# Kernel tuning notes

Measured on AMD Instinct MI355X. Metric: run time of the kernel, lower is better.

## Reference

```python
import jax, jax.numpy as jnp
import numpy as np

B, S, C, HD = 2, 4096, 2048, 128
H = C // HD  # 16 heads
EPS = 1.1920929e-07  # torch RMSNorm default eps for float32 (finfo.eps)


def _make_rope(seq_len, head_dim):
    # Standard RoPE 2x2 rotation matrices: [1, S, 1, head_dim//2, 2, 2]
    half = head_dim // 2
    freqs = 1.0 / (10000.0 ** (np.arange(0, half, dtype=np.float32) / half))
    ang = np.arange(seq_len, dtype=np.float32)[:, None] * freqs[None, :]  # [S, half]
    cos, sin = np.cos(ang), np.sin(ang)
    rot = np.stack([np.stack([cos, -sin], axis=-1),
                    np.stack([sin, cos], axis=-1)], axis=-2)  # [S, half, 2, 2]
    return jnp.asarray(rot[None, :, None])  # [1, S, 1, half, 2, 2]


def setup_inputs() -> dict:
    key = jax.random.key(0)
    ks = jax.random.split(key, 9)
    sc = 1.0 / np.sqrt(C)
    return {
        "x": jax.random.normal(ks[0], (B, S, C), jnp.float32),
        "rope": _make_rope(S, HD),
        "wq": jax.random.normal(ks[1], (C, C), jnp.float32) * sc,
        "bq": jax.random.normal(ks[2], (C,), jnp.float32) * 0.01,
        "wk": jax.random.normal(ks[3], (C, C), jnp.float32) * sc,
        "bk": jax.random.normal(ks[4], (C,), jnp.float32) * 0.01,
        "wv": jax.random.normal(ks[5], (C, C), jnp.float32) * sc,
        "bv": jax.random.normal(ks[6], (C,), jnp.float32) * 0.01,
        "q_norm_w": jnp.ones((HD,), jnp.float32),
        "k_norm_w": jnp.ones((HD,), jnp.float32),
    }


def _rmsnorm(t, w):
    t32 = t.astype(jnp.float32)
    inv = jax.lax.rsqrt(jnp.mean(t32 * t32, axis=-1, keepdims=True) + EPS)
    return (t32 * inv * w).astype(t.dtype)


def _apply_rotary(t, rope):
    # t: [B, S, H, HD] -> pairs [B, S, H, HD//2, 1, 2]; rope: [1, S, 1, HD//2, 2, 2]
    t32 = t.reshape(*t.shape[:-1], HD // 2, 1, 2).astype(jnp.float32)
    out = (rope * t32).sum(axis=-1)  # [B, S, H, HD//2, 2]
    return out.reshape(t.shape).astype(t.dtype)


def reference(x, rope, wq, bq, wk, bk, wv, bv, q_norm_w, k_norm_w):
    # QKV projections (torch Linear: x @ W^T + b)
    q = (jnp.einsum('bsc,oc->bso', x, wq) + bq).reshape(B, S, H, HD)
    k = (jnp.einsum('bsc,oc->bso', x, wk) + bk).reshape(B, S, H, HD)
    v = (jnp.einsum('bsc,oc->bso', x, wv) + bv).reshape(B, S, H, HD)
    # Per-head RMSNorm on q, k (in float32, cast back), then rotary
    q = _apply_rotary(_rmsnorm(q, q_norm_w), rope)
    k = _apply_rotary(_rmsnorm(k, k_norm_w), rope)
    return (q, k, v)
```

## Files before the change

### kernel.cpp

```cpp
#include <hip/hip_runtime.h>


#define M_DIM 8192
#define N_DIM 6144
#define K_DIM 2048
#define NKT 32
#define EPS_RMS 1.1920929e-07f

typedef __bf16 bf16x8 __attribute__((ext_vector_type(8)));
typedef float f32x4 __attribute__((ext_vector_type(4)));

__device__ __forceinline__ void gload16(const void* g, void* l) {
  __builtin_amdgcn_global_load_lds(
      (const __attribute__((address_space(1))) unsigned int*)g,
      (__attribute__((address_space(3))) unsigned int*)l, 16, 0, 0);
}

__device__ __forceinline__ unsigned short f2bf(float f) {
  union { float f; unsigned u; } x; x.f = f;
  unsigned r = x.u + 0x7FFFu + ((x.u >> 16) & 1u);
  return (unsigned short)(r >> 16);
}

__global__ void __launch_bounds__(256) cvt_kernel(const float* __restrict__ s,
                                                  unsigned short* __restrict__ d, int n4) {
  int i = blockIdx.x * blockDim.x + threadIdx.x;
  const int stride = gridDim.x * blockDim.x;
  for (; i < n4; i += stride) {
    const float4 v = reinterpret_cast<const float4*>(s)[i];
    ushort4 o;
    o.x = f2bf(v.x); o.y = f2bf(v.y); o.z = f2bf(v.z); o.w = f2bf(v.w);
    reinterpret_cast<ushort4*>(d)[i] = o;
  }
}

#define LDS4(ARR, BASE, OFF) (*(const f32x4*)((const char*)(ARR) + (BASE) + (OFF)))

#define SGB_DS(N)   __builtin_amdgcn_sched_group_barrier(0x100, (N), 0)
#define SGB_MFMA(N) __builtin_amdgcn_sched_group_barrier(0x8, (N), 0)

#define MFMA_PH(MH, NH)                                                              \
  {                                                                                  \
    _Pragma("unroll")                                                                \
    for (int mf4 = 0; mf4 < 4; ++mf4) {                                              \
      _Pragma("unroll")                                                              \
      for (int nf2 = 0; nf2 < 2; ++nf2) {                                            \
        f32x4& c = acc[(MH) * 4 + mf4][(NH) * 2 + nf2];                              \
        c = __builtin_amdgcn_mfma_f32_16x16x32_bf16(                                 \
            __builtin_bit_cast(bf16x8, Af[mf4][0]),                                  \
            __builtin_bit_cast(bf16x8, Bf[NH][nf2][0]), c, 0, 0, 0);                 \
        c = __builtin_amdgcn_mfma_f32_16x16x32_bf16(                                 \
            __builtin_bit_cast(bf16x8, Af[mf4][1]),                                  \
            __builtin_bit_cast(bf16x8, Bf[NH][nf2][1]), c, 0, 0, 0);                 \
      }                                                                              \
    }                                                                                \
  }

__global__ void __launch_bounds__(512, 2) gemm_fused(
    const unsigned short* __restrict__ xbf, const unsigned short* __restrict__ wbf,
    const float* __restrict__ rope,
    const float* __restrict__ bq, const float* __restrict__ bk, const float* __restrict__ bv,
    const float* __restrict__ qnw, const float* __restrict__ knw,
    float* __restrict__ dout) {
  const int id = blockIdx.x;
  const int xcd = id & 7;
  const int j = id >> 3;
  const int bm = (xcd << 2) | (j & 3);
  const int bn = j >> 2;
  const int m0 = bm << 8, n0 = bn << 8;
  const int tid = threadIdx.x;
  const int w = tid >> 6, l = tid & 63;
  const int l15 = l & 15, lhi = l >> 4;
  const int wr = w >> 2, wc = w & 3;

  __shared__ __align__(16) unsigned short As[32768];
  __shared__ __align__(16) unsigned short Bs[32768];

  const int srow = tid >> 3;
  const int schunk = (tid & 7) ^ (srow & 7);
  const unsigned short* aSrc = xbf + ((size_t)(m0 + srow) << 11) + (schunk << 3);
  const unsigned short* bSrc = wbf + ((size_t)(n0 + srow) << 11) + (schunk << 3);
  char* aDst = (char*)As + (w << 10);
  char* bDst = (char*)Bs + (w << 10);

#define STA(KT, Q) gload16(aSrc + ((size_t)(Q) << 17) + ((KT) << 6), aDst + ((((KT) & 1) << 15) + ((Q) << 13)))
#define STB(KT, Q) gload16(bSrc + ((size_t)(Q) << 17) + ((KT) << 6), bDst + ((((KT) & 1) << 15) + ((Q) << 13)))

  const int sl0 = ((lhi ^ (l15 & 7)) << 4);
  const int sl1 = (((lhi + 4) ^ (l15 & 7)) << 4);
  unsigned a0 = (wr << 14) + (l15 << 7) + sl0;
  unsigned a1 = (wr << 14) + (l15 << 7) + sl1;
  unsigned b0 = (wc << 13) + (l15 << 7) + sl0;
  unsigned b1 = (wc << 13) + (l15 << 7) + sl1;

  f32x4 acc[8][4];
#pragma unroll
  for (int i = 0; i < 8; ++i)
#pragma unroll
    for (int jj = 0; jj < 4; ++jj) acc[i][jj] = (f32x4){0.f, 0.f, 0.f, 0.f};

  f32x4 Af[4][2];
  f32x4 Bf[2][2][2];

  STA(0, 0); STA(0, 2);
  STB(0, 0); STB(0, 1); STB(0, 2); STB(0, 3);
  STA(0, 1); STA(0, 3);
  asm volatile("s_waitcnt vmcnt(2)" ::: "memory");
  __builtin_amdgcn_s_barrier();
  asm volatile("" ::: "memory");

  for (int kt = 0; kt < NKT; ++kt) {
    const bool notLast = (kt < NKT - 1);
    Af[0][0] = LDS4(As, a0, 0);        Af[0][1] = LDS4(As, a1, 0);
    Bf[0][0][0] = LDS4(Bs, b0, 0);     Bf[0][0][1] = LDS4(Bs, b1, 0);
    Bf[0][1][0] = LDS4(Bs, b0, 2048);  Bf[0][1][1] = LDS4(Bs, b1, 2048);
    Af[1][0] = LDS4(As, a0, 2048);     Af[1][1] = LDS4(As, a1, 2048);
    Af[2][0] = LDS4(As, a0, 4096);     Af[2][1] = LDS4(As, a1, 4096);
    Af[3][0] = LDS4(As, a0, 6144);     Af[3][1] = LDS4(As, a1, 6144);
    Bf[1][0][0] = LDS4(Bs, b0, 4096);  Bf[1][0][1] = LDS4(Bs, b1, 4096);
    Bf[1][1][0] = LDS4(Bs, b0, 6144);  Bf[1][1][1] = LDS4(Bs, b1, 6144);
    if (notLast) {
      STA(kt + 1, 0); STA(kt + 1, 2);
      STB(kt + 1, 0); STB(kt + 1, 1); STB(kt + 1, 2); STB(kt + 1, 3);
    }
    __builtin_amdgcn_s_setprio(1);
    MFMA_PH(0, 0);
    MFMA_PH(0, 1);
    SGB_DS(4);  SGB_MFMA(2);
    SGB_DS(2);  SGB_MFMA(2);
    SGB_DS(2);  SGB_MFMA(4);
    SGB_DS(2);  SGB_MFMA(4);
    SGB_DS(2);  SGB_MFMA(4);
    SGB_DS(4);  SGB_MFMA(16);
    __builtin_amdgcn_s_setprio(0);
    if (notLast) { asm volatile("s_waitcnt vmcnt(6)" ::: "memory"); }
    else         { asm volatile("s_waitcnt vmcnt(0)" ::: "memory"); }
    __builtin_amdgcn_s_barrier();
    asm volatile("" ::: "memory");
    Af[0][0] = LDS4(As, a0, 8192);  Af[0][1] = LDS4(As, a1, 8192);
    Af[1][0] = LDS4(As, a0, 10240); Af[1][1] = LDS4(As, a1, 10240);
    Af[2][0] = LDS4(As, a0, 12288); Af[2][1] = LDS4(As, a1, 12288);
    Af[3][0] = LDS4(As, a0, 14336); Af[3][1] = LDS4(As, a1, 14336);
    if (notLast) { STA(kt + 1, 1); STA(kt + 1, 3); }
    __builtin_amdgcn_s_setprio(1);
    MFMA_PH(1, 0);
    MFMA_PH(1, 1);
    SGB_DS(2);  SGB_MFMA(4);
    SGB_DS(2);  SGB_MFMA(4);
    SGB_DS(2);  SGB_MFMA(4);
    SGB_DS(2);  SGB_MFMA(4);
    SGB_MFMA(16);
    __builtin_amdgcn_s_setprio(0);
    if (notLast) { asm volatile("s_waitcnt vmcnt(2)" ::: "memory"); }
    __builtin_amdgcn_s_barrier();
    asm volatile("" ::: "memory");
    a0 ^= 32768u; a1 ^= 32768u; b0 ^= 32768u; b1 ^= 32768u;
  }

  float* scr = (float*)As;
  const int sec = bn >> 3;
  const int nsec = (n0 & 2047) + (wc << 6);
  const float* bias = sec == 0 ? bq : (sec == 1 ? bk : bv);
  float biasv[4];
#pragma unroll
  for (int nf = 0; nf < 4; ++nf) biasv[nf] = bias[nsec + nf * 16 + l15];
  const size_t outBase = ((size_t)sec << 24);

  if (sec < 2) {
    const float* nwp = sec ? knw : qnw;
    const int colh = (wc & 1) << 6;
    float nwv[4];
#pragma unroll
    for (int nf = 0; nf < 4; ++nf) nwv[nf] = nwp[colh + nf * 16 + l15];
    float ssv[8][4];
#pragma unroll
    for (int mf = 0; mf < 8; ++mf) {
#pragma unroll
      for (int jj = 0; jj < 4; ++jj) {
        float ss = 0.f;
#pragma unroll
        for (int nf = 0; nf < 4; ++nf) {
          const float t = acc[mf][nf][jj] + biasv[nf];
          ss += t * t;
        }
        ss += __shfl_xor(ss, 1);
        ss += __shfl_xor(ss, 2);
        ss += __shfl_xor(ss, 4);
        ss += __shfl_xor(ss, 8);
        ssv[mf][jj] = ss;
      }
    }
    if (l15 == 0) {
#pragma unroll
      for (int mf = 0; mf < 8; ++mf)
#pragma unroll
        for (int jj = 0; jj < 4; ++jj)
          scr[(w << 7) + mf * 16 + (lhi << 2) + jj] = ssv[mf][jj];
    }
    __syncthreads();
#pragma unroll
    for (int mf = 0; mf < 8; ++mf) {
#pragma unroll
      for (int jj = 0; jj < 4; ++jj) {
        const float tot = ssv[mf][jj] + scr[((w ^ 1) << 7) + mf * 16 + (lhi << 2) + jj];
        const float inv = rsqrtf(tot * (1.0f / 128.0f) + EPS_RMS);
        const int m = m0 + (wr << 7) + mf * 16 + (lhi << 2) + jj;
        const float* rp = rope + ((size_t)(m & 4095) << 8);
        float* orow = dout + outBase + ((size_t)m << 11) + nsec + l15;
#pragma unroll
        for (int nf = 0; nf < 4; ++nf) {
          const float tn = (acc[mf][nf][jj] + biasv[nf]) * inv * nwv[nf];
          const float pn = __shfl_xor(tn, 1);
          const int ch = colh + nf * 16 + l15;
          const int jr = ch >> 1;
          const float o = fmaf(rp[jr << 2], tn, rp[(jr << 2) + 1 + (ch & 1)] * pn);
          orow[nf << 4] = o;
        }
      }
    }
  } else {
#pragma unroll
    for (int mf = 0; mf < 8; ++mf)
#pragma unroll
      for (int jj = 0; jj < 4; ++jj) {
        const int m = m0 + (wr << 7) + mf * 16 + (lhi << 2) + jj;
        float* orow = dout + outBase + ((size_t)m << 11) + nsec + l15;
#pragma unroll
        for (int nf = 0; nf < 4; ++nf) orow[nf << 4] = acc[mf][nf][jj] + biasv[nf];
      }
  }
}

extern "C" void kernel_launch(void* const* d_in, const int* in_sizes, int n_in,
                              void* d_out, int out_size, void* d_ws, size_t ws_size,
                              hipStream_t stream) {
  const float* x = (const float*)d_in[0];
  const float* rope = (const float*)d_in[1];
  const float* wq = (const float*)d_in[2];
  const float* bq = (const float*)d_in[3];
  const float* wk = (const float*)d_in[4];
  const float* bk = (const float*)d_in[5];
  const float* wv = (const float*)d_in[6];
  const float* bv = (const float*)d_in[7];
  const float* qnw = (const float*)d_in[8];
  const float* knw = (const float*)d_in[9];

  unsigned short* xbf = (unsigned short*)d_ws;
  unsigned short* wbf = xbf + (size_t)M_DIM * K_DIM;

  cvt_kernel<<<2048, 256, 0, stream>>>(x, xbf, M_DIM * K_DIM / 4);
  cvt_kernel<<<1024, 256, 0, stream>>>(wq, wbf, K_DIM * K_DIM / 4);
  cvt_kernel<<<1024, 256, 0, stream>>>(wk, wbf + (size_t)K_DIM * K_DIM, K_DIM * K_DIM / 4);
  cvt_kernel<<<1024, 256, 0, stream>>>(wv, wbf + (size_t)2 * K_DIM * K_DIM, K_DIM * K_DIM / 4);

  gemm_fused<<<(M_DIM / 256) * (N_DIM / 256), 512, 0, stream>>>(
      xbf, wbf, rope, bq, bk, bv, qnw, knw, (float*)d_out);
}
```

Before: 240.3 us.

## Restructure GEMM main loop into four k-half phases with split B layout

```diff
diff --git a/kernel.cpp b/kernel.cpp
--- a/kernel.cpp
+++ b/kernel.cpp
@@ -34,27 +34,22 @@
   }
 }
 
-#define LDS4(ARR, BASE, OFF) (*(const f32x4*)((const char*)(ARR) + (BASE) + (OFF)))
-
-#define SGB_DS(N)   __builtin_amdgcn_sched_group_barrier(0x100, (N), 0)
-#define SGB_MFMA(N) __builtin_amdgcn_sched_group_barrier(0x8, (N), 0)
-
-#define MFMA_PH(MH, NH)                                                              \
+#define LDS4(ARR, OFF) (*(const f32x4*)((const char*)(ARR) + (OFF)))
+
+#define MFMA16(MH)                                                                   \
   {                                                                                  \
     _Pragma("unroll")                                                                \
     for (int mf4 = 0; mf4 < 4; ++mf4) {                                              \
       _Pragma("unroll")                                                              \
-      for (int nf2 = 0; nf2 < 2; ++nf2) {                                            \
-        f32x4& c = acc[(MH) * 4 + mf4][(NH) * 2 + nf2];                              \
-        c = __builtin_amdgcn_mfma_f32_16x16x32_bf16(                                 \
-            __builtin_bit_cast(bf16x8, Af[mf4][0]),                                  \
-            __builtin_bit_cast(bf16x8, Bf[NH][nf2][0]), c, 0, 0, 0);                 \
-        c = __builtin_amdgcn_mfma_f32_16x16x32_bf16(                                 \
-            __builtin_bit_cast(bf16x8, Af[mf4][1]),                                  \
-            __builtin_bit_cast(bf16x8, Bf[NH][nf2][1]), c, 0, 0, 0);                 \
+      for (int nf4 = 0; nf4 < 4; ++nf4) {                                            \
+        acc[(MH) * 4 + mf4][nf4] = __builtin_amdgcn_mfma_f32_16x16x32_bf16(          \
+            __builtin_bit_cast(bf16x8, Af[mf4]),                                     \
+            __builtin_bit_cast(bf16x8, Bf[nf4]), acc[(MH) * 4 + mf4][nf4], 0, 0, 0); \
       }                                                                              \
     }                                                                                \
   }
+
+#define FENCE asm volatile("" ::: "memory")
 
 __global__ void __launch_bounds__(512, 2) gemm_fused(
     const unsigned short* __restrict__ xbf, const unsigned short* __restrict__ wbf,
@@ -64,9 +59,9 @@
     float* __restrict__ dout) {
   const int id = blockIdx.x;
   const int xcd = id & 7;
-  const int j = id >> 3;
-  const int bm = (xcd << 2) | (j & 3);
-  const int bn = j >> 2;
+  const int jb = id >> 3;
+  const int bm = (xcd << 2) | (jb & 3);
+  const int bn = jb >> 2;
   const int m0 = bm << 8, n0 = bn << 8;
   const int tid = threadIdx.x;
   const int w = tid >> 6, l = tid & 63;
@@ -76,22 +71,26 @@
   __shared__ __align__(16) unsigned short As[32768];
   __shared__ __align__(16) unsigned short Bs[32768];
 
-  const int srow = tid >> 3;
-  const int schunk = (tid & 7) ^ (srow & 7);
-  const unsigned short* aSrc = xbf + ((size_t)(m0 + srow) << 11) + (schunk << 3);
-  const unsigned short* bSrc = wbf + ((size_t)(n0 + srow) << 11) + (schunk << 3);
+  const int cA = (tid & 7) ^ ((tid >> 3) & 7);
+  const unsigned short* aSrc = xbf + ((size_t)(m0 + (tid >> 3)) << 11) + (cA << 3);
   char* aDst = (char*)As + (w << 10);
+#define STA(KT, Q) gload16(aSrc + ((size_t)(Q) << 17) + ((KT) << 6), aDst + ((((KT) & 1) << 15) + ((Q) << 13)))
+
+  const int cB = (tid & 3) ^ ((tid >> 3) & 3);
+  const unsigned short* bSrc = wbf + ((size_t)(n0 + (tid >> 2)) << 11) + (cB << 3);
   char* bDst = (char*)Bs + (w << 10);
-
-#define STA(KT, Q) gload16(aSrc + ((size_t)(Q) << 17) + ((KT) << 6), aDst + ((((KT) & 1) << 15) + ((Q) << 13)))
-#define STB(KT, Q) gload16(bSrc + ((size_t)(Q) << 17) + ((KT) << 6), bDst + ((((KT) & 1) << 15) + ((Q) << 13)))
+#define STB(KT, KH)                                                                        \
+  do {                                                                                     \
+    gload16(bSrc + ((KT) << 6) + ((KH) << 5), bDst + ((((KT) & 1) << 15) + ((KH) << 14))); \
+    gload16(bSrc + ((size_t)128 << 11) + ((KT) << 6) + ((KH) << 5),                        \
+            bDst + ((((KT) & 1) << 15) + ((KH) << 14)) + 8192);                            \
+  } while (0)
 
   const int sl0 = ((lhi ^ (l15 & 7)) << 4);
   const int sl1 = (((lhi + 4) ^ (l15 & 7)) << 4);
-  unsigned a0 = (wr << 14) + (l15 << 7) + sl0;
-  unsigned a1 = (wr << 14) + (l15 << 7) + sl1;
-  unsigned b0 = (wc << 13) + (l15 << 7) + sl0;
-  unsigned b1 = (wc << 13) + (l15 << 7) + sl1;
+  const unsigned aB0 = (unsigned)((wr << 14) + (l15 << 7) + sl0);
+  const unsigned aB1 = (unsigned)((wr << 14) + (l15 << 7) + sl1);
+  const unsigned bB = (unsigned)((wc << 12) + (l15 << 6) + ((lhi ^ ((l15 >> 1) & 3)) << 4));
 
   f32x4 acc[8][4];
 #pragma unroll
@@ -99,62 +98,70 @@
 #pragma unroll
     for (int jj = 0; jj < 4; ++jj) acc[i][jj] = (f32x4){0.f, 0.f, 0.f, 0.f};
 
-  f32x4 Af[4][2];
-  f32x4 Bf[2][2][2];
-
+  f32x4 Af[4];
+  f32x4 Bf[4];
+
+  STB(0, 0);
   STA(0, 0); STA(0, 2);
-  STB(0, 0); STB(0, 1); STB(0, 2); STB(0, 3);
   STA(0, 1); STA(0, 3);
-  asm volatile("s_waitcnt vmcnt(2)" ::: "memory");
+  STB(0, 1);
+  asm volatile("s_waitcnt vmcnt(4)" ::: "memory");
   __builtin_amdgcn_s_barrier();
-  asm volatile("" ::: "memory");
-
+  FENCE;
+
+  unsigned abuf = 0, bbuf = 0;
   for (int kt = 0; kt < NKT; ++kt) {
-    const bool notLast = (kt < NKT - 1);
-    Af[0][0] = LDS4(As, a0, 0);        Af[0][1] = LDS4(As, a1, 0);
-    Bf[0][0][0] = LDS4(Bs, b0, 0);     Bf[0][0][1] = LDS4(Bs, b1, 0);
-    Bf[0][1][0] = LDS4(Bs, b0, 2048);  Bf[0][1][1] = LDS4(Bs, b1, 2048);
-    Af[1][0] = LDS4(As, a0, 2048);     Af[1][1] = LDS4(As, a1, 2048);
-    Af[2][0] = LDS4(As, a0, 4096);     Af[2][1] = LDS4(As, a1, 4096);
-    Af[3][0] = LDS4(As, a0, 6144);     Af[3][1] = LDS4(As, a1, 6144);
-    Bf[1][0][0] = LDS4(Bs, b0, 4096);  Bf[1][0][1] = LDS4(Bs, b1, 4096);
-    Bf[1][1][0] = LDS4(Bs, b0, 6144);  Bf[1][1][1] = LDS4(Bs, b1, 6144);
-    if (notLast) {
-      STA(kt + 1, 0); STA(kt + 1, 2);
-      STB(kt + 1, 0); STB(kt + 1, 1); STB(kt + 1, 2); STB(kt + 1, 3);
-    }
-    __builtin_amdgcn_s_setprio(1);
-    MFMA_PH(0, 0);
-    MFMA_PH(0, 1);
-    SGB_DS(4);  SGB_MFMA(2);
-    SGB_DS(2);  SGB_MFMA(2);
-    SGB_DS(2);  SGB_MFMA(4);
-    SGB_DS(2);  SGB_MFMA(4);
-    SGB_DS(2);  SGB_MFMA(4);
-    SGB_DS(4);  SGB_MFMA(16);
-    __builtin_amdgcn_s_setprio(0);
-    if (notLast) { asm volatile("s_waitcnt vmcnt(6)" ::: "memory"); }
-    else         { asm volatile("s_waitcnt vmcnt(0)" ::: "memory"); }
-    __builtin_amdgcn_s_barrier();
-    asm volatile("" ::: "memory");
-    Af[0][0] = LDS4(As, a0, 8192);  Af[0][1] = LDS4(As, a1, 8192);
-    Af[1][0] = LDS4(As, a0, 10240); Af[1][1] = LDS4(As, a1, 10240);
-    Af[2][0] = LDS4(As, a0, 12288); Af[2][1] = LDS4(As, a1, 12288);
-    Af[3][0] = LDS4(As, a0, 14336); Af[3][1] = LDS4(As, a1, 14336);
-    if (notLast) { STA(kt + 1, 1); STA(kt + 1, 3); }
-    __builtin_amdgcn_s_setprio(1);
-    MFMA_PH(1, 0);
-    MFMA_PH(1, 1);
-    SGB_DS(2);  SGB_MFMA(4);
-    SGB_DS(2);  SGB_MFMA(4);
-    SGB_DS(2);  SGB_MFMA(4);
-    SGB_DS(2);  SGB_MFMA(4);
-    SGB_MFMA(16);
-    __builtin_amdgcn_s_setprio(0);
-    if (notLast) { asm volatile("s_waitcnt vmcnt(2)" ::: "memory"); }
-    __builtin_amdgcn_s_barrier();
-    asm volatile("" ::: "memory");
-    a0 ^= 32768u; a1 ^= 32768u; b0 ^= 32768u; b1 ^= 32768u;
+    const bool nl = (kt < NKT - 1);
+    Af[0] = LDS4(As, abuf + aB0);        Af[1] = LDS4(As, abuf + aB0 + 2048);
+    Af[2] = LDS4(As, abuf + aB0 + 4096); Af[3] = LDS4(As, abuf + aB0 + 6144);
+    Bf[0] = LDS4(Bs, bbuf + bB);         Bf[1] = LDS4(Bs, bbuf + bB + 1024);
+    Bf[2] = LDS4(Bs, bbuf + bB + 2048);  Bf[3] = LDS4(Bs, bbuf + bB + 3072);
+    if (nl) STB(kt + 1, 0);
+    __builtin_amdgcn_s_barrier();
+    FENCE;
+    __builtin_amdgcn_s_setprio(1);
+    MFMA16(0);
+    __builtin_amdgcn_s_setprio(0);
+    if (nl) { asm volatile("s_waitcnt vmcnt(4)" ::: "memory"); }
+    else    { asm volatile("s_waitcnt vmcnt(2)" ::: "memory"); }
+    __builtin_amdgcn_s_barrier();
+    FENCE;
+    Af[0] = LDS4(As, abuf + aB0 + 8192);  Af[1] = LDS4(As, abuf + aB0 + 10240);
+    Af[2] = LDS4(As, abuf + aB0 + 12288); Af[3] = LDS4(As, abuf + aB0 + 14336);
+    if (nl) { STA(kt + 1, 0); STA(kt + 1, 2); }
+    __builtin_amdgcn_s_barrier();
+    FENCE;
+    __builtin_amdgcn_s_setprio(1);
+    MFMA16(1);
+    __builtin_amdgcn_s_setprio(0);
+    if (nl) { asm volatile("s_waitcnt vmcnt(4)" ::: "memory"); }
+    else    { asm volatile("s_waitcnt vmcnt(0)" ::: "memory"); }
+    __builtin_amdgcn_s_barrier();
+    FENCE;
+    Af[0] = LDS4(As, abuf + aB1 + 8192);  Af[1] = LDS4(As, abuf + aB1 + 10240);
+    Af[2] = LDS4(As, abuf + aB1 + 12288); Af[3] = LDS4(As, abuf + aB1 + 14336);
+    Bf[0] = LDS4(Bs, bbuf + bB + 16384);  Bf[1] = LDS4(Bs, bbuf + bB + 17408);
+    Bf[2] = LDS4(Bs, bbuf + bB + 18432);  Bf[3] = LDS4(Bs, bbuf + bB + 19456);
+    if (nl) { STA(kt + 1, 1); STA(kt + 1, 3); }
+    __builtin_amdgcn_s_barrier();
+    FENCE;
+    __builtin_amdgcn_s_setprio(1);
+    MFMA16(1);
+    __builtin_amdgcn_s_setprio(0);
+    __builtin_amdgcn_s_barrier();
+    FENCE;
+    Af[0] = LDS4(As, abuf + aB1);        Af[1] = LDS4(As, abuf + aB1 + 2048);
+    Af[2] = LDS4(As, abuf + aB1 + 4096); Af[3] = LDS4(As, abuf + aB1 + 6144);
+    if (nl) STB(kt + 1, 1);
+    __builtin_amdgcn_s_barrier();
+    FENCE;
+    __builtin_amdgcn_s_setprio(1);
+    MFMA16(0);
+    __builtin_amdgcn_s_setprio(0);
+    if (nl) { asm volatile("s_waitcnt vmcnt(4)" ::: "memory"); }
+    __builtin_amdgcn_s_barrier();
+    FENCE;
+    abuf ^= 32768u; bbuf ^= 32768u;
   }
 
   float* scr = (float*)As;
```

New measurement: 264.9 us. 10.2% more time.

## Simplify GEMM main loop to one barrier per k-tile with upfront prefetch

Applied to the files above, without the earlier changes.

```diff
diff --git a/kernel.cpp b/kernel.cpp
--- a/kernel.cpp
+++ b/kernel.cpp
@@ -35,9 +35,6 @@
 }
 
 #define LDS4(ARR, BASE, OFF) (*(const f32x4*)((const char*)(ARR) + (BASE) + (OFF)))
-
-#define SGB_DS(N)   __builtin_amdgcn_sched_group_barrier(0x100, (N), 0)
-#define SGB_MFMA(N) __builtin_amdgcn_sched_group_barrier(0x8, (N), 0)
 
 #define MFMA_PH(MH, NH)                                                              \
   {                                                                                  \
@@ -56,6 +53,8 @@
     }                                                                                \
   }
 
+#define FENCE asm volatile("" ::: "memory")
+
 __global__ void __launch_bounds__(512, 2) gemm_fused(
     const unsigned short* __restrict__ xbf, const unsigned short* __restrict__ wbf,
     const float* __restrict__ rope,
@@ -64,9 +63,9 @@
     float* __restrict__ dout) {
   const int id = blockIdx.x;
   const int xcd = id & 7;
-  const int j = id >> 3;
-  const int bm = (xcd << 2) | (j & 3);
-  const int bn = j >> 2;
+  const int jb = id >> 3;
+  const int bm = (xcd << 2) | (jb & 3);
+  const int bn = jb >> 2;
   const int m0 = bm << 8, n0 = bn << 8;
   const int tid = threadIdx.x;
   const int w = tid >> 6, l = tid & 63;
@@ -102,15 +101,18 @@
   f32x4 Af[4][2];
   f32x4 Bf[2][2][2];
 
-  STA(0, 0); STA(0, 2);
+  STA(0, 0); STA(0, 1); STA(0, 2); STA(0, 3);
   STB(0, 0); STB(0, 1); STB(0, 2); STB(0, 3);
-  STA(0, 1); STA(0, 3);
-  asm volatile("s_waitcnt vmcnt(2)" ::: "memory");
+  asm volatile("s_waitcnt vmcnt(0)" ::: "memory");
   __builtin_amdgcn_s_barrier();
-  asm volatile("" ::: "memory");
+  FENCE;
 
   for (int kt = 0; kt < NKT; ++kt) {
     const bool notLast = (kt < NKT - 1);
+    if (notLast) {
+      STA(kt + 1, 0); STA(kt + 1, 1); STA(kt + 1, 2); STA(kt + 1, 3);
+      STB(kt + 1, 0); STB(kt + 1, 1); STB(kt + 1, 2); STB(kt + 1, 3);
+    }
     Af[0][0] = LDS4(As, a0, 0);        Af[0][1] = LDS4(As, a1, 0);
     Bf[0][0][0] = LDS4(Bs, b0, 0);     Bf[0][0][1] = LDS4(Bs, b1, 0);
     Bf[0][1][0] = LDS4(Bs, b0, 2048);  Bf[0][1][1] = LDS4(Bs, b1, 2048);
@@ -119,41 +121,21 @@
     Af[3][0] = LDS4(As, a0, 6144);     Af[3][1] = LDS4(As, a1, 6144);
     Bf[1][0][0] = LDS4(Bs, b0, 4096);  Bf[1][0][1] = LDS4(Bs, b1, 4096);
     Bf[1][1][0] = LDS4(Bs, b0, 6144);  Bf[1][1][1] = LDS4(Bs, b1, 6144);
-    if (notLast) {
-      STA(kt + 1, 0); STA(kt + 1, 2);
-      STB(kt + 1, 0); STB(kt + 1, 1); STB(kt + 1, 2); STB(kt + 1, 3);
-    }
     __builtin_amdgcn_s_setprio(1);
     MFMA_PH(0, 0);
     MFMA_PH(0, 1);
-    SGB_DS(4);  SGB_MFMA(2);
-    SGB_DS(2);  SGB_MFMA(2);
-    SGB_DS(2);  SGB_MFMA(4);
-    SGB_DS(2);  SGB_MFMA(4);
-    SGB_DS(2);  SGB_MFMA(4);
-    SGB_DS(4);  SGB_MFMA(16);
     __builtin_amdgcn_s_setprio(0);
-    if (notLast) { asm volatile("s_waitcnt vmcnt(6)" ::: "memory"); }
-    else         { asm volatile("s_waitcnt vmcnt(0)" ::: "memory"); }
-    __builtin_amdgcn_s_barrier();
-    asm volatile("" ::: "memory");
     Af[0][0] = LDS4(As, a0, 8192);  Af[0][1] = LDS4(As, a1, 8192);
     Af[1][0] = LDS4(As, a0, 10240); Af[1][1] = LDS4(As, a1, 10240);
     Af[2][0] = LDS4(As, a0, 12288); Af[2][1] = LDS4(As, a1, 12288);
     Af[3][0] = LDS4(As, a0, 14336); Af[3][1] = LDS4(As, a1, 14336);
-    if (notLast) { STA(kt + 1, 1); STA(kt + 1, 3); }
     __builtin_amdgcn_s_setprio(1);
     MFMA_PH(1, 0);
     MFMA_PH(1, 1);
-    SGB_DS(2);  SGB_MFMA(4);
-    SGB_DS(2);  SGB_MFMA(4);
-    SGB_DS(2);  SGB_MFMA(4);
-    SGB_DS(2);  SGB_MFMA(4);
-    SGB_MFMA(16);
     __builtin_amdgcn_s_setprio(0);
-    if (notLast) { asm volatile("s_waitcnt vmcnt(2)" ::: "memory"); }
+    asm volatile("s_waitcnt vmcnt(0)" ::: "memory");
     __builtin_amdgcn_s_barrier();
-    asm volatile("" ::: "memory");
+    FENCE;
     a0 ^= 32768u; a1 ^= 32768u; b0 ^= 32768u; b1 ^= 32768u;
   }
 
```

New measurement: 269.8 us. 1.12x slower.
